# Optimization experiments

Hardware: AMD Instinct MI355X
Metric: run time of the kernel (lower is better)

The kernel has to match this reference:

```python
import jax, jax.numpy as jnp
import numpy as np

Z_DIM = 64
HIDDEN = 400
DATASET = 1000000
EPS = 0.01
S_STEPS = 20
T_STEPS = 5
LOG_2PI = float(np.log(2.0 * np.pi))


def setup_inputs() -> dict:
    key = jax.random.key(0)
    ks = jax.random.split(key, 10)
    B = 16384
    x = jax.random.uniform(ks[0], (B, 1, 28, 28), dtype=jnp.float32)
    indices = jax.random.randint(ks[1], (B,), 0, DATASET, dtype=jnp.int64)
    # MLP params (torch Linear convention: y = x @ W.T + b)
    W1 = jax.random.normal(ks[2], (HIDDEN, 784), dtype=jnp.float32) * 0.03
    b1 = jnp.zeros((HIDDEN,), dtype=jnp.float32)
    W21 = jax.random.normal(ks[3], (Z_DIM, HIDDEN), dtype=jnp.float32) * 0.05
    b21 = jnp.zeros((Z_DIM,), dtype=jnp.float32)
    W22 = jax.random.normal(ks[4], (Z_DIM, HIDDEN), dtype=jnp.float32) * 0.05
    b22 = jnp.zeros((Z_DIM,), dtype=jnp.float32)
    cached_samples = jax.random.normal(ks[5], (DATASET, Z_DIM), dtype=jnp.float32)
    # pre-drawn Langevin noise for all s+t steps
    noise = jax.random.normal(ks[6], (S_STEPS + T_STEPS, B, Z_DIM), dtype=jnp.float32)
    return {"x": x, "indices": indices, "K": 1, "W1": W1, "b1": b1,
            "W21": W21, "b21": b21, "W22": W22, "b22": b22,
            "cached_samples": cached_samples, "noise": noise}


def _encode(x, W1, b1, W21, b21, W22, b22):
    xf = x.reshape(-1, 784)
    h = jax.nn.relu(xf @ W1.T + b1)
    z_loc = h @ W21.T + b21
    z_scale = jnp.exp(h @ W22.T + b22)
    return z_loc, z_scale


def _langevin(z0, noise_steps, z_loc, z_scale):
    # ULA: z <- z + eps * grad_log_q(z) + sqrt(2*eps) * xi
    inv_var = 1.0 / (z_scale * z_scale)
    coef = jnp.sqrt(2.0 * EPS).astype(z0.dtype)

    def step(z, xi):
        grad = (z_loc - z) * inv_var
        return z + EPS * grad + coef * xi, None

    z, _ = jax.lax.scan(step, z0, noise_steps)
    return z


def reference(x, indices, K, W1, b1, W21, b21, W22, b22, cached_samples, noise):
    z_loc, z_scale = _encode(x, W1, b1, W21, b21, W22, b22)
    # gather cached particles
    z = cached_samples[indices]
    # s detached steps, then t graph-carrying steps (same math in fwd)
    z = jax.lax.stop_gradient(_langevin(z, noise[:S_STEPS], z_loc, z_scale))
    z = _langevin(z, noise[S_STEPS:], z_loc, z_scale)
    # scatter updated particles back
    new_cache = cached_samples.at[indices].set(jax.lax.stop_gradient(z))
    # Normal log-prob summed over latent dim
    log_qz_x = jnp.sum(
        -0.5 * jnp.square((z - z_loc) / z_scale) - jnp.log(z_scale) - 0.5 * LOG_2PI,
        axis=-1)
    return log_qz_x, z, new_cache
```

## Files before the change

kernel.cpp:

```cpp
#include <hip/hip_runtime.h>


#define ZD 64
#define NSTEPS 25
#define EPSI 0.01f
#define K1 784
#define K1P 800
#define HSTR 512
#define COPYB 2048

typedef __attribute__((ext_vector_type(8))) short short8;
typedef __attribute__((ext_vector_type(4))) float f32x4;
typedef __attribute__((ext_vector_type(4))) int i32x4;

__device__ __forceinline__ unsigned short f2bf(float f) {
  union { float f; unsigned u; } v; v.f = f;
  return (unsigned short)((v.u + 0x7FFFu + ((v.u >> 16) & 1u)) >> 16);
}

__device__ __forceinline__ void gload_lds16(const void* g, void* l) {
  __builtin_amdgcn_global_load_lds(
      (const __attribute__((address_space(1))) void*)g,
      (__attribute__((address_space(3))) void*)l, 16, 0, 0);
}

__global__ __launch_bounds__(256) void prep_kernel(
    const float* __restrict__ W1, const float* __restrict__ W21,
    const float* __restrict__ W22, short* __restrict__ W1b,
    short* __restrict__ Wout) {
  const int t = blockIdx.x * 256 + threadIdx.x;
  const int NW1 = 512 * (K1P / 8);
  if (t < NW1) {
    const int n = t / (K1P / 8), k0 = (t % (K1P / 8)) * 8;
    short8 v = {0, 0, 0, 0, 0, 0, 0, 0};
    if (n < 400 && k0 < K1) {
      const float* s = W1 + (long)n * K1 + k0;
#pragma unroll
      for (int e = 0; e < 8; e++) v[e] = (short)f2bf(s[e]);
    }
    *(short8*)(W1b + (long)t * 8) = v;
  } else {
    const int q = t - NW1;
    if (q < 128 * 64) {
      const int n = q / 64, k0 = (q % 64) * 8;
      short8 v = {0, 0, 0, 0, 0, 0, 0, 0};
      if (k0 < 400) {
        const float* s = (n < 64) ? (W21 + (long)n * 400 + k0)
                                  : (W22 + (long)(n - 64) * 400 + k0);
#pragma unroll
        for (int e = 0; e < 8; e++) v[e] = (short)f2bf(s[e]);
      }
      *(short8*)(Wout + (long)q * 8) = v;
    }
  }
}

__global__ __launch_bounds__(256) void zero_win_kernel(i32x4* __restrict__ win4, int n4) {
  const int t = blockIdx.x * 256 + threadIdx.x;
  if (t < n4) win4[t] = (i32x4){0, 0, 0, 0};
}

__global__ __launch_bounds__(256) void winner_kernel(
    const int* __restrict__ idx, int* __restrict__ winner, int B) {
  const int j = blockIdx.x * 256 + threadIdx.x;
  if (j < B) atomicMax(&winner[idx[j]], j + 1);
}

__global__ __launch_bounds__(256) void gemm1_copy_kernel(
    const float* __restrict__ X, const short* __restrict__ W1b,
    const float* __restrict__ b1, unsigned short* __restrict__ H,
    const f32x4* __restrict__ cache4, f32x4* __restrict__ out4,
    int ngemm, long n4) {
  __shared__ short As[2 * 64 * 8];
  __shared__ short Bs[32 * 64 * 8];
  const int tid = threadIdx.x;

  if ((int)blockIdx.x >= ngemm) {
    const long base = (long)(blockIdx.x - ngemm) * (256 * 32) + tid;
#pragma unroll
    for (int k = 0; k < 32; k++) {
      const long e = base + (long)k * 256;
      if (e < n4) {
        f32x4 v = __builtin_nontemporal_load(&cache4[e]);
        __builtin_nontemporal_store(v, &out4[e]);
      }
    }
    return;
  }

  const int w = tid >> 6;
  const int lane = tid & 63;
  const int m0 = blockIdx.x * 32;

  const f32x4 vzero = {0.f, 0.f, 0.f, 0.f};
  f32x4 acc[2][8];
#pragma unroll
  for (int i = 0; i < 2; i++)
#pragma unroll
    for (int j = 0; j < 8; j++) acc[i][j] = vzero;

  for (int k0 = 0; k0 < K1P; k0 += 32) {
    if (k0) __syncthreads();
    if (tid < 128) {
      const int row = m0 + (tid >> 6) * 16 + (lane & 15);
      const int gk = k0 + (lane >> 4) * 8;
      short8 av = {0, 0, 0, 0, 0, 0, 0, 0};
      if (gk < K1) {
        const float4 f0 = *(const float4*)(X + (long)row * K1 + gk);
        const float4 f1 = *(const float4*)(X + (long)row * K1 + gk + 4);
        av[0] = (short)f2bf(f0.x); av[1] = (short)f2bf(f0.y);
        av[2] = (short)f2bf(f0.z); av[3] = (short)f2bf(f0.w);
        av[4] = (short)f2bf(f1.x); av[5] = (short)f2bf(f1.y);
        av[6] = (short)f2bf(f1.z); av[7] = (short)f2bf(f1.w);
      }
      *(short8*)(As + (long)tid * 8) = av;
    }
#pragma unroll
    for (int t = 0; t < 8; t++) {
      const int gn = w * 8 + t;
      const short* src = W1b + (long)(gn * 16 + (lane & 15)) * K1P +
                         k0 + (lane >> 4) * 8;
      gload_lds16(src, Bs + gn * 512);
    }
    __syncthreads();
    const short8* Ap = (const short8*)As;
    const short8* Bp = (const short8*)Bs;
    const short8 a0 = Ap[0 * 64 + lane];
    const short8 a1 = Ap[1 * 64 + lane];
#pragma unroll
    for (int j = 0; j < 8; j++) {
      const short8 b = Bp[(w * 8 + j) * 64 + lane];
      acc[0][j] = __builtin_amdgcn_mfma_f32_16x16x32_bf16(a0, b, acc[0][j], 0, 0, 0);
      acc[1][j] = __builtin_amdgcn_mfma_f32_16x16x32_bf16(a1, b, acc[1][j], 0, 0, 0);
    }
  }
  const int colg = lane & 15;
  const int rowg = (lane >> 4) * 4;
#pragma unroll
  for (int j = 0; j < 8; j++) {
    const int col = w * 128 + j * 16 + colg;
    const float bias = (col < 400) ? b1[col] : 0.f;
#pragma unroll
    for (int i = 0; i < 2; i++) {
      const int rbase = m0 + i * 16 + rowg;
#pragma unroll
      for (int r = 0; r < 4; r++) {
        H[(long)(rbase + r) * HSTR + col] = f2bf(fmaxf(acc[i][j][r] + bias, 0.f));
      }
    }
  }
}

__global__ __launch_bounds__(256) void gemm2_kernel(
    const unsigned short* __restrict__ H, const short* __restrict__ Wout,
    const float* __restrict__ b21, const float* __restrict__ b22,
    float* __restrict__ zloc, float* __restrict__ uarr) {
  __shared__ short As[2 * 64 * 8];
  __shared__ short Bs[8 * 64 * 8];
  const int tid = threadIdx.x;
  const int w = tid >> 6;
  const int lane = tid & 63;
  const int m0 = blockIdx.x * 32;

  const f32x4 vzero = {0.f, 0.f, 0.f, 0.f};
  f32x4 acc[2][2];
#pragma unroll
  for (int i = 0; i < 2; i++)
#pragma unroll
    for (int j = 0; j < 2; j++) acc[i][j] = vzero;

  for (int k0 = 0; k0 < HSTR; k0 += 32) {
    if (k0) __syncthreads();
    if (w < 2) {
      const unsigned short* src = H + (long)(m0 + w * 16 + (lane & 15)) * HSTR +
                                  k0 + (lane >> 4) * 8;
      gload_lds16(src, As + w * 512);
    }
#pragma unroll
    for (int t = 0; t < 2; t++) {
      const int gn = w * 2 + t;
      const short* src = Wout + (long)(gn * 16 + (lane & 15)) * HSTR +
                         k0 + (lane >> 4) * 8;
      gload_lds16(src, Bs + gn * 512);
    }
    __syncthreads();
    const short8* Ap = (const short8*)As;
    const short8* Bp = (const short8*)Bs;
    const short8 a0 = Ap[0 * 64 + lane];
    const short8 a1 = Ap[1 * 64 + lane];
#pragma unroll
    for (int j = 0; j < 2; j++) {
      const short8 b = Bp[(w * 2 + j) * 64 + lane];
      acc[0][j] = __builtin_amdgcn_mfma_f32_16x16x32_bf16(a0, b, acc[0][j], 0, 0, 0);
      acc[1][j] = __builtin_amdgcn_mfma_f32_16x16x32_bf16(a1, b, acc[1][j], 0, 0, 0);
    }
  }
  const int colg = lane & 15;
  const int rowg = (lane >> 4) * 4;
  float* outp = (w < 2) ? zloc : uarr;
  const float* bp = (w < 2) ? b21 : b22;
#pragma unroll
  for (int j = 0; j < 2; j++) {
    const int col = (w & 1) * 32 + j * 16 + colg;
    const float bias = bp[col];
#pragma unroll
    for (int i = 0; i < 2; i++) {
      const int rbase = m0 + i * 16 + rowg;
#pragma unroll
      for (int r = 0; r < 4; r++) {
        outp[(long)(rbase + r) * ZD + col] = acc[i][j][r] + bias;
      }
    }
  }
}

__global__ __launch_bounds__(256) void langevin_kernel(
    const float* __restrict__ zloc, const float* __restrict__ uarr,
    const float* __restrict__ cache, const int* __restrict__ idx,
    const float* __restrict__ noise, const int* __restrict__ winner,
    float* __restrict__ out_logq, float* __restrict__ out_z,
    float* __restrict__ out_cache, int B) {
  const int row = blockIdx.x * 4 + (threadIdx.x >> 6);
  const int lane = threadIdx.x & 63;
  const int i = idx[row];
  const float zl = zloc[(long)row * ZD + lane];
  const float uu = uarr[(long)row * ZD + lane];
  const float a = EPSI * expf(-2.f * uu);
  float z = cache[(long)i * ZD + lane];
  const float coef = sqrtf(2.f * EPSI);
  const float* np = noise + (long)row * ZD + lane;
  const long stride = (long)B * ZD;
#pragma unroll
  for (int s = 0; s < NSTEPS; s++) {
    z = z + a * (zl - z) + coef * np[(long)s * stride];
  }
  out_z[(long)row * ZD + lane] = z;
  if (winner[i] == row + 1) {
    out_cache[(long)i * ZD + lane] = z;
  }
  const float d = (z - zl) * expf(-uu);
  float t = -0.5f * d * d - uu - 0.91893853320467274178f;
#pragma unroll
  for (int off = 1; off < 64; off <<= 1) t += __shfl_xor(t, off);
  if (lane == 0) out_logq[row] = t;
}

extern "C" void kernel_launch(void* const* d_in, const int* in_sizes, int n_in,
                              void* d_out, int out_size, void* d_ws, size_t ws_size,
                              hipStream_t stream) {
  const float* x     = (const float*)d_in[0];
  const int*   idx   = (const int*)d_in[1];
  const float* W1    = (const float*)d_in[3];
  const float* b1    = (const float*)d_in[4];
  const float* W21   = (const float*)d_in[5];
  const float* b21   = (const float*)d_in[6];
  const float* W22   = (const float*)d_in[7];
  const float* b22   = (const float*)d_in[8];
  const float* cache = (const float*)d_in[9];
  const float* noise = (const float*)d_in[10];

  const int B  = in_sizes[1];
  const int DS = in_sizes[9] / ZD;

  float* out_logq  = (float*)d_out;
  float* out_z     = out_logq + B;
  float* out_cache = out_z + (long)B * ZD;

  unsigned short* h = (unsigned short*)d_ws;
  short* w1b  = (short*)(h + (long)B * HSTR);
  short* wout = w1b + 512 * K1P;
  float* zloc = (float*)(wout + 128 * HSTR);
  float* u    = zloc + (long)B * ZD;
  int*   win  = (int*)(u + (long)B * ZD);

  const int n4i = (DS + 3) / 4;
  zero_win_kernel<<<(n4i + 255) / 256, 256, 0, stream>>>((i32x4*)win, n4i);

  const int prep_chunks = 512 * (K1P / 8) + 128 * 64;
  prep_kernel<<<(prep_chunks + 255) / 256, 256, 0, stream>>>(W1, W21, W22, w1b, wout);
  winner_kernel<<<(B + 255) / 256, 256, 0, stream>>>(idx, win, B);

  const int ngemm = B / 32;
  const long total4 = (long)DS * (ZD / 4);
  gemm1_copy_kernel<<<ngemm + COPYB, 256, 0, stream>>>(
      x, w1b, b1, h, (const f32x4*)cache, (f32x4*)out_cache, ngemm, total4);

  gemm2_kernel<<<B / 32, 256, 0, stream>>>(h, wout, b21, b22, zloc, u);
  langevin_kernel<<<B / 4, 256, 0, stream>>>(zloc, u, cache, idx, noise, win,
                                             out_logq, out_z, out_cache, B);
}
```

Measured before the change: 191.2 us.

## Split cache copy across all three kernels and halve gemm1 N-tile

Splits the 256 MB cache-to-output copy into three portions that run as extra blocks inside gemm1, gemm2 and the Langevin kernel, so the bandwidth-bound copy overlaps each compute stage. The copy now skips rows that the Langevin kernel will overwrite, using the winner array, so later scatter writes cannot be clobbered by copy blocks in the same launch. gemm1 now splits N into two 256-column halves, which doubles the GEMM block count and halves LDS use. The cost is a winner lookup per 16-byte element, plain (cached) loads in place of nontemporal ones, and a single element per thread instead of 32 per block.

Result: no change. 192.0 us (+0.4%).

```diff
diff --git a/kernel.cpp b/kernel.cpp
--- a/kernel.cpp
+++ b/kernel.cpp
@@ -7,7 +7,6 @@
 #define K1 784
 #define K1P 800
 #define HSTR 512
-#define COPYB 2048
 
 typedef __attribute__((ext_vector_type(8))) short short8;
 typedef __attribute__((ext_vector_type(4))) float f32x4;
@@ -22,6 +21,19 @@
   __builtin_amdgcn_global_load_lds(
       (const __attribute__((address_space(1))) void*)g,
       (__attribute__((address_space(3))) void*)l, 16, 0, 0);
+}
+
+__device__ __forceinline__ void copy_role(const f32x4* __restrict__ cache4,
+                                          const int* __restrict__ winner,
+                                          f32x4* __restrict__ out4,
+                                          long e, long n4) {
+  if (e < n4) {
+    const long row = e >> 4;
+    if (winner[row] == 0) {
+      f32x4 v = cache4[e];
+      __builtin_nontemporal_store(v, &out4[e]);
+    }
+  }
 }
 
 __global__ __launch_bounds__(256) void prep_kernel(
@@ -69,35 +81,29 @@
 __global__ __launch_bounds__(256) void gemm1_copy_kernel(
     const float* __restrict__ X, const short* __restrict__ W1b,
     const float* __restrict__ b1, unsigned short* __restrict__ H,
-    const f32x4* __restrict__ cache4, f32x4* __restrict__ out4,
-    int ngemm, long n4) {
+    const f32x4* __restrict__ cache4, const int* __restrict__ winner,
+    f32x4* __restrict__ out4, int ngemm, long cbase, long n4) {
   __shared__ short As[2 * 64 * 8];
-  __shared__ short Bs[32 * 64 * 8];
+  __shared__ short Bs[16 * 64 * 8];
   const int tid = threadIdx.x;
 
   if ((int)blockIdx.x >= ngemm) {
-    const long base = (long)(blockIdx.x - ngemm) * (256 * 32) + tid;
-#pragma unroll
-    for (int k = 0; k < 32; k++) {
-      const long e = base + (long)k * 256;
-      if (e < n4) {
-        f32x4 v = __builtin_nontemporal_load(&cache4[e]);
-        __builtin_nontemporal_store(v, &out4[e]);
-      }
-    }
+    const long e = cbase + (long)(blockIdx.x - ngemm) * 256 + tid;
+    copy_role(cache4, winner, out4, e, n4);
     return;
   }
 
   const int w = tid >> 6;
   const int lane = tid & 63;
-  const int m0 = blockIdx.x * 32;
+  const int m0 = (blockIdx.x >> 1) * 32;
+  const int n0 = (blockIdx.x & 1) * 256;
 
   const f32x4 vzero = {0.f, 0.f, 0.f, 0.f};
-  f32x4 acc[2][8];
+  f32x4 acc[2][4];
 #pragma unroll
   for (int i = 0; i < 2; i++)
 #pragma unroll
-    for (int j = 0; j < 8; j++) acc[i][j] = vzero;
+    for (int j = 0; j < 4; j++) acc[i][j] = vzero;
 
   for (int k0 = 0; k0 < K1P; k0 += 32) {
     if (k0) __syncthreads();
@@ -116,9 +122,9 @@
       *(short8*)(As + (long)tid * 8) = av;
     }
 #pragma unroll
-    for (int t = 0; t < 8; t++) {
-      const int gn = w * 8 + t;
-      const short* src = W1b + (long)(gn * 16 + (lane & 15)) * K1P +
+    for (int t = 0; t < 4; t++) {
+      const int gn = w * 4 + t;
+      const short* src = W1b + (long)(n0 + gn * 16 + (lane & 15)) * K1P +
                          k0 + (lane >> 4) * 8;
       gload_lds16(src, Bs + gn * 512);
     }
@@ -128,8 +134,8 @@
     const short8 a0 = Ap[0 * 64 + lane];
     const short8 a1 = Ap[1 * 64 + lane];
 #pragma unroll
-    for (int j = 0; j < 8; j++) {
-      const short8 b = Bp[(w * 8 + j) * 64 + lane];
+    for (int j = 0; j < 4; j++) {
+      const short8 b = Bp[(w * 4 + j) * 64 + lane];
       acc[0][j] = __builtin_amdgcn_mfma_f32_16x16x32_bf16(a0, b, acc[0][j], 0, 0, 0);
       acc[1][j] = __builtin_amdgcn_mfma_f32_16x16x32_bf16(a1, b, acc[1][j], 0, 0, 0);
     }
@@ -137,8 +143,8 @@
   const int colg = lane & 15;
   const int rowg = (lane >> 4) * 4;
 #pragma unroll
-  for (int j = 0; j < 8; j++) {
-    const int col = w * 128 + j * 16 + colg;
+  for (int j = 0; j < 4; j++) {
+    const int col = n0 + w * 64 + j * 16 + colg;
     const float bias = (col < 400) ? b1[col] : 0.f;
 #pragma unroll
     for (int i = 0; i < 2; i++) {
@@ -151,13 +157,22 @@
   }
 }
 
-__global__ __launch_bounds__(256) void gemm2_kernel(
+__global__ __launch_bounds__(256) void gemm2_copy_kernel(
     const unsigned short* __restrict__ H, const short* __restrict__ Wout,
     const float* __restrict__ b21, const float* __restrict__ b22,
-    float* __restrict__ zloc, float* __restrict__ uarr) {
+    float* __restrict__ zloc, float* __restrict__ uarr,
+    const f32x4* __restrict__ cache4, const int* __restrict__ winner,
+    f32x4* __restrict__ out4, int ngemm, long cbase, long n4) {
   __shared__ short As[2 * 64 * 8];
   __shared__ short Bs[8 * 64 * 8];
   const int tid = threadIdx.x;
+
+  if ((int)blockIdx.x >= ngemm) {
+    const long e = cbase + (long)(blockIdx.x - ngemm) * 256 + tid;
+    copy_role(cache4, winner, out4, e, n4);
+    return;
+  }
+
   const int w = tid >> 6;
   const int lane = tid & 63;
   const int m0 = blockIdx.x * 32;
@@ -214,14 +229,22 @@
   }
 }
 
-__global__ __launch_bounds__(256) void langevin_kernel(
+__global__ __launch_bounds__(256) void langevin_copy_kernel(
     const float* __restrict__ zloc, const float* __restrict__ uarr,
     const float* __restrict__ cache, const int* __restrict__ idx,
     const float* __restrict__ noise, const int* __restrict__ winner,
     float* __restrict__ out_logq, float* __restrict__ out_z,
-    float* __restrict__ out_cache, int B) {
-  const int row = blockIdx.x * 4 + (threadIdx.x >> 6);
-  const int lane = threadIdx.x & 63;
+    float* __restrict__ out_cache, int B, int nlan, long cbase, long n4) {
+  const int tid = threadIdx.x;
+
+  if ((int)blockIdx.x >= nlan) {
+    const long e = cbase + (long)(blockIdx.x - nlan) * 256 + tid;
+    copy_role((const f32x4*)cache, winner, (f32x4*)out_cache, e, n4);
+    return;
+  }
+
+  const int row = blockIdx.x * 4 + (tid >> 6);
+  const int lane = tid & 63;
   const int i = idx[row];
   const float zl = zloc[(long)row * ZD + lane];
   const float uu = uarr[(long)row * ZD + lane];
@@ -280,12 +303,24 @@
   prep_kernel<<<(prep_chunks + 255) / 256, 256, 0, stream>>>(W1, W21, W22, w1b, wout);
   winner_kernel<<<(B + 255) / 256, 256, 0, stream>>>(idx, win, B);
 
-  const int ngemm = B / 32;
-  const long total4 = (long)DS * (ZD / 4);
-  gemm1_copy_kernel<<<ngemm + COPYB, 256, 0, stream>>>(
-      x, w1b, b1, h, (const f32x4*)cache, (f32x4*)out_cache, ngemm, total4);
-
-  gemm2_kernel<<<B / 32, 256, 0, stream>>>(h, wout, b21, b22, zloc, u);
-  langevin_kernel<<<B / 4, 256, 0, stream>>>(zloc, u, cache, idx, noise, win,
-                                             out_logq, out_z, out_cache, B);
-}
+  const long n4 = (long)DS * (ZD / 4);
+  const int ncpy = (int)(n4 / 256);
+  const int c1 = 32768;
+  const int c2 = 8192;
+  const int c3 = ncpy - c1 - c2;
+
+  const int ngemm1 = (B / 32) * 2;
+  gemm1_copy_kernel<<<ngemm1 + c1, 256, 0, stream>>>(
+      x, w1b, b1, h, (const f32x4*)cache, win, (f32x4*)out_cache,
+      ngemm1, 0L, n4);
+
+  const int ngemm2 = B / 32;
+  gemm2_copy_kernel<<<ngemm2 + c2, 256, 0, stream>>>(
+      h, wout, b21, b22, zloc, u, (const f32x4*)cache, win,
+      (f32x4*)out_cache, ngemm2, (long)c1 * 256, n4);
+
+  const int nlan = B / 4;
+  langevin_copy_kernel<<<nlan + c3, 256, 0, stream>>>(
+      zloc, u, cache, idx, noise, win, out_logq, out_z, out_cache,
+      B, nlan, (long)(c1 + c2) * 256, n4);
+}
```

## Split fused gemm1/copy, halve gemm1 N tile, zero only touched winner slots

Applied to the files above, without the earlier changes.

Pulls the 256MB cache copy out of the gemm1 kernel into its own plain copy kernel, launched after gemm2, and drops the nontemporal hints. gemm1 now splits the N dimension across two blocks per row tile, which doubles the grid and halves the LDS footprint. The full zeroing of the million-entry winner array is replaced by zeroing only the slots that idx touches. The change loses the overlap between the copy and the GEMM work, and the copy kernel assumes DS*16 is divisible by 256.

Measured after the change: 200.1 us. 1.05x slower.

```diff
diff --git a/kernel.cpp b/kernel.cpp
--- a/kernel.cpp
+++ b/kernel.cpp
@@ -7,11 +7,9 @@
 #define K1 784
 #define K1P 800
 #define HSTR 512
-#define COPYB 2048
 
 typedef __attribute__((ext_vector_type(8))) short short8;
 typedef __attribute__((ext_vector_type(4))) float f32x4;
-typedef __attribute__((ext_vector_type(4))) int i32x4;
 
 __device__ __forceinline__ unsigned short f2bf(float f) {
   union { float f; unsigned u; } v; v.f = f;
@@ -55,9 +53,10 @@
   }
 }
 
-__global__ __launch_bounds__(256) void zero_win_kernel(i32x4* __restrict__ win4, int n4) {
-  const int t = blockIdx.x * 256 + threadIdx.x;
-  if (t < n4) win4[t] = (i32x4){0, 0, 0, 0};
+__global__ __launch_bounds__(256) void zero_touched_kernel(
+    const int* __restrict__ idx, int* __restrict__ winner, int B) {
+  const int j = blockIdx.x * 256 + threadIdx.x;
+  if (j < B) winner[idx[j]] = 0;
 }
 
 __global__ __launch_bounds__(256) void winner_kernel(
@@ -66,38 +65,23 @@
   if (j < B) atomicMax(&winner[idx[j]], j + 1);
 }
 
-__global__ __launch_bounds__(256) void gemm1_copy_kernel(
+__global__ __launch_bounds__(256) void gemm1_kernel(
     const float* __restrict__ X, const short* __restrict__ W1b,
-    const float* __restrict__ b1, unsigned short* __restrict__ H,
-    const f32x4* __restrict__ cache4, f32x4* __restrict__ out4,
-    int ngemm, long n4) {
+    const float* __restrict__ b1, unsigned short* __restrict__ H) {
   __shared__ short As[2 * 64 * 8];
-  __shared__ short Bs[32 * 64 * 8];
+  __shared__ short Bs[16 * 64 * 8];
   const int tid = threadIdx.x;
-
-  if ((int)blockIdx.x >= ngemm) {
-    const long base = (long)(blockIdx.x - ngemm) * (256 * 32) + tid;
-#pragma unroll
-    for (int k = 0; k < 32; k++) {
-      const long e = base + (long)k * 256;
-      if (e < n4) {
-        f32x4 v = __builtin_nontemporal_load(&cache4[e]);
-        __builtin_nontemporal_store(v, &out4[e]);
-      }
-    }
-    return;
-  }
-
   const int w = tid >> 6;
   const int lane = tid & 63;
-  const int m0 = blockIdx.x * 32;
+  const int m0 = (blockIdx.x >> 1) * 32;
+  const int n0 = (blockIdx.x & 1) * 256;
 
   const f32x4 vzero = {0.f, 0.f, 0.f, 0.f};
-  f32x4 acc[2][8];
+  f32x4 acc[2][4];
 #pragma unroll
   for (int i = 0; i < 2; i++)
 #pragma unroll
-    for (int j = 0; j < 8; j++) acc[i][j] = vzero;
+    for (int j = 0; j < 4; j++) acc[i][j] = vzero;
 
   for (int k0 = 0; k0 < K1P; k0 += 32) {
     if (k0) __syncthreads();
@@ -116,9 +100,9 @@
       *(short8*)(As + (long)tid * 8) = av;
     }
 #pragma unroll
-    for (int t = 0; t < 8; t++) {
-      const int gn = w * 8 + t;
-      const short* src = W1b + (long)(gn * 16 + (lane & 15)) * K1P +
+    for (int t = 0; t < 4; t++) {
+      const int gn = w * 4 + t;
+      const short* src = W1b + (long)(n0 + gn * 16 + (lane & 15)) * K1P +
                          k0 + (lane >> 4) * 8;
       gload_lds16(src, Bs + gn * 512);
     }
@@ -128,8 +112,8 @@
     const short8 a0 = Ap[0 * 64 + lane];
     const short8 a1 = Ap[1 * 64 + lane];
 #pragma unroll
-    for (int j = 0; j < 8; j++) {
-      const short8 b = Bp[(w * 8 + j) * 64 + lane];
+    for (int j = 0; j < 4; j++) {
+      const short8 b = Bp[(w * 4 + j) * 64 + lane];
       acc[0][j] = __builtin_amdgcn_mfma_f32_16x16x32_bf16(a0, b, acc[0][j], 0, 0, 0);
       acc[1][j] = __builtin_amdgcn_mfma_f32_16x16x32_bf16(a1, b, acc[1][j], 0, 0, 0);
     }
@@ -137,8 +121,8 @@
   const int colg = lane & 15;
   const int rowg = (lane >> 4) * 4;
 #pragma unroll
-  for (int j = 0; j < 8; j++) {
-    const int col = w * 128 + j * 16 + colg;
+  for (int j = 0; j < 4; j++) {
+    const int col = n0 + w * 64 + j * 16 + colg;
     const float bias = (col < 400) ? b1[col] : 0.f;
 #pragma unroll
     for (int i = 0; i < 2; i++) {
@@ -212,6 +196,12 @@
       }
     }
   }
+}
+
+__global__ __launch_bounds__(256) void copy_kernel(
+    const f32x4* __restrict__ src, f32x4* __restrict__ dst) {
+  const long e = (long)blockIdx.x * 256 + threadIdx.x;
+  dst[e] = src[e];
 }
 
 __global__ __launch_bounds__(256) void langevin_kernel(
@@ -273,19 +263,18 @@
   float* u    = zloc + (long)B * ZD;
   int*   win  = (int*)(u + (long)B * ZD);
 
-  const int n4i = (DS + 3) / 4;
-  zero_win_kernel<<<(n4i + 255) / 256, 256, 0, stream>>>((i32x4*)win, n4i);
-
   const int prep_chunks = 512 * (K1P / 8) + 128 * 64;
   prep_kernel<<<(prep_chunks + 255) / 256, 256, 0, stream>>>(W1, W21, W22, w1b, wout);
+  zero_touched_kernel<<<(B + 255) / 256, 256, 0, stream>>>(idx, win, B);
   winner_kernel<<<(B + 255) / 256, 256, 0, stream>>>(idx, win, B);
 
-  const int ngemm = B / 32;
-  const long total4 = (long)DS * (ZD / 4);
-  gemm1_copy_kernel<<<ngemm + COPYB, 256, 0, stream>>>(
-      x, w1b, b1, h, (const f32x4*)cache, (f32x4*)out_cache, ngemm, total4);
-
+  gemm1_kernel<<<(B / 32) * 2, 256, 0, stream>>>(x, w1b, b1, h);
   gemm2_kernel<<<B / 32, 256, 0, stream>>>(h, wout, b21, b22, zloc, u);
+
+  const long n4 = (long)DS * (ZD / 4);
+  copy_kernel<<<(unsigned)(n4 / 256), 256, 0, stream>>>(
+      (const f32x4*)cache, (f32x4*)out_cache);
+
   langevin_kernel<<<B / 4, 256, 0, stream>>>(zloc, u, cache, idx, noise, win,
                                              out_logq, out_z, out_cache, B);
 }
```
